# Kernel tuning notes

Measured on AMD Instinct MI355X. Metric: run time of the kernel, lower is better.

Reference implementation:

```python
import jax, jax.numpy as jnp
import numpy as np
from jax import lax

B, L, D, NH, EL, PL, CIN, DFF, NTF = 64, 512, 128, 8, 2, 96, 8, 2048, 4
EPS = 1e-5

def _pos_encoding(seq_len, d):
    pos = np.arange(seq_len, dtype=np.float32)[:, None]
    div = np.exp(np.arange(0, d, 2, dtype=np.float32) * -(np.log(10000.0) / d))
    pe = np.zeros((seq_len, d), dtype=np.float32)
    pe[:, 0::2] = np.sin(pos * div)
    pe[:, 1::2] = np.cos(pos * div)
    return jnp.asarray(pe)

def _layernorm(x, g, b):
    mu = x.mean(-1, keepdims=True)
    var = ((x - mu) ** 2).mean(-1, keepdims=True)
    return (x - mu) * lax.rsqrt(var + EPS) * g + b

def setup_inputs() -> dict:
    key = jax.random.key(0)
    ks = iter(jax.random.split(key, 40))
    s = 0.02
    inp = {
        'x_enc': jax.random.normal(next(ks), (B, L, CIN), jnp.float32),
        'x_mark_enc': jax.random.normal(next(ks), (B, L, NTF), jnp.float32),
        'x_dec': jax.random.normal(next(ks), (B, PL, CIN), jnp.float32),
        'x_mark_dec': jax.random.normal(next(ks), (B, PL, NTF), jnp.float32),
        'conv_w': jax.random.normal(next(ks), (D, CIN, 3), jnp.float32) * s,
        'temp_w': jax.random.normal(next(ks), (D, NTF), jnp.float32) * s,
        'lstm_Wih': jax.random.normal(next(ks), (4 * D, D), jnp.float32) * s,
        'lstm_Whh': jax.random.normal(next(ks), (4 * D, D), jnp.float32) * s,
        'lstm_bih': jnp.zeros((4 * D,), jnp.float32),
        'lstm_bhh': jnp.zeros((4 * D,), jnp.float32),
        'Wqkv': jax.random.normal(next(ks), (EL, 3 * D, D), jnp.float32) * s,
        'bqkv': jnp.zeros((EL, 3 * D), jnp.float32),
        'Wo': jax.random.normal(next(ks), (EL, D, D), jnp.float32) * s,
        'bo': jnp.zeros((EL, D), jnp.float32),
        'ln1g': jnp.ones((EL, D), jnp.float32),
        'ln1b': jnp.zeros((EL, D), jnp.float32),
        'W1': jax.random.normal(next(ks), (EL, DFF, D), jnp.float32) * s,
        'b1': jnp.zeros((EL, DFF), jnp.float32),
        'W2': jax.random.normal(next(ks), (EL, D, DFF), jnp.float32) * s,
        'b2': jnp.zeros((EL, D), jnp.float32),
        'ln2g': jnp.ones((EL, D), jnp.float32),
        'ln2b': jnp.zeros((EL, D), jnp.float32),
        'head_w': jax.random.normal(next(ks), (PL, D), jnp.float32) * s,
        'head_b': jnp.zeros((PL,), jnp.float32),
        'gate_w1': jax.random.normal(next(ks), (D // 2, D), jnp.float32) * s,
        'gate_b1': jnp.zeros((D // 2,), jnp.float32),
        'gate_w2': jax.random.normal(next(ks), (PL, D // 2), jnp.float32) * s,
        'gate_b2': jnp.zeros((PL,), jnp.float32),
        'g_omega': jnp.array([0.01], jnp.float32),
        'g_alpha': jnp.array([-2.0], jnp.float32),
        'g_beta': jnp.array([1.0], jnp.float32),
        'g_h0': jnp.array([0.1], jnp.float32),
    }
    return inp

def reference(x_enc, x_mark_enc, x_dec, x_mark_dec, conv_w, temp_w,
              lstm_Wih, lstm_Whh, lstm_bih, lstm_bhh,
              Wqkv, bqkv, Wo, bo, ln1g, ln1b, W1, b1, W2, b2, ln2g, ln2b,
              head_w, head_b, gate_w1, gate_b1, gate_w2, gate_b2,
              g_omega, g_alpha, g_beta, g_h0):
    # ---- NeuralGARCH: scalar linear recurrence over seq, then pred rollout ----
    returns = x_enc[:, :, -2]                       # [B, L]
    omega = jax.nn.softplus(g_omega[0])
    alpha = jax.nn.sigmoid(g_alpha[0]) * 0.2
    beta = jax.nn.sigmoid(g_beta[0]) * 0.8
    h0 = jnp.broadcast_to(jax.nn.softplus(g_h0[0]), (B,))
    def g_step(h, r):
        return omega + alpha * r ** 2 + beta * h, None
    h_last, _ = lax.scan(g_step, h0, returns.T)     # scan over L
    def f_step(h, _):
        return omega + (alpha + beta) * h, h
    _, hs = lax.scan(f_step, h_last, None, length=PL)   # [PL, B]
    garch_pred = jnp.sqrt(hs.T)                     # [B, PL]
    # ---- DataEmbedding: circular conv1d + temporal linear + positional ----
    xc = jnp.transpose(x_enc, (0, 2, 1))            # [B, CIN, L]
    xp = jnp.pad(xc, ((0, 0), (0, 0), (1, 1)), mode='wrap')
    val = lax.conv_general_dilated(xp, conv_w, (1,), 'VALID',
                                   dimension_numbers=('NCH', 'OIH', 'NCH'))
    val = jnp.transpose(val, (0, 2, 1))             # [B, L, D]
    enc = val + x_mark_enc @ temp_w.T + _pos_encoding(L, D)[None]
    # ---- single-layer LSTM (gate order i,f,g,o) ----
    xW = enc @ lstm_Wih.T + lstm_bih + lstm_bhh     # [B, L, 4D]
    def l_step(carry, xw_t):
        h, c = carry
        g = xw_t + h @ lstm_Whh.T
        i, f, gg, o = jnp.split(g, 4, axis=-1)
        c = jax.nn.sigmoid(f) * c + jax.nn.sigmoid(i) * jnp.tanh(gg)
        h = jax.nn.sigmoid(o) * jnp.tanh(c)
        return (h, c), h
    init = (jnp.zeros((B, D), enc.dtype), jnp.zeros((B, D), enc.dtype))
    _, hseq = lax.scan(l_step, init, jnp.transpose(xW, (1, 0, 2)))
    x = jnp.transpose(hseq, (1, 0, 2))              # [B, L, D]
    # ---- TransformerEncoder (post-norm, relu) ----
    dh = D // NH
    for li in range(EL):
        qkv = x @ Wqkv[li].T + bqkv[li]
        q, k, v = jnp.split(qkv, 3, axis=-1)
        q = q.reshape(B, L, NH, dh).transpose(0, 2, 1, 3)
        k = k.reshape(B, L, NH, dh).transpose(0, 2, 1, 3)
        v = v.reshape(B, L, NH, dh).transpose(0, 2, 1, 3)
        scores = jnp.einsum('bhqd,bhkd->bhqk', q, k) / jnp.sqrt(jnp.float32(dh))
        attn = jax.nn.softmax(scores, axis=-1)
        ctx = jnp.einsum('bhqk,bhkd->bhqd', attn, v)
        ctx = ctx.transpose(0, 2, 1, 3).reshape(B, L, D)
        x = _layernorm(x + ctx @ Wo[li].T + bo[li], ln1g[li], ln1b[li])
        ff = jax.nn.relu(x @ W1[li].T + b1[li]) @ W2[li].T + b2[li]
        x = _layernorm(x + ff, ln2g[li], ln2b[li])
    last = x[:, -1, :]                              # [B, D]
    ai_residual = last @ head_w.T + head_b          # [B, PL]
    gate = jax.nn.sigmoid(jax.nn.relu(last @ gate_w1.T + gate_b1) @ gate_w2.T + gate_b2)
    final = garch_pred + gate * ai_residual
    return final[..., None]                         # [B, PL, 1]
```

## Files before the change

### kernel.cpp

```cpp
#include <hip/hip_runtime.h>
#include <hip/hip_bf16.h>
#include <math.h>

#define Bn 64
#define Lq 512
#define Dm 128
#define NHh 8
#define ELn 2
#define PLn 96
#define CINn 8
#define DFFn 2048
#define NTFn 4
#define EPSf 1e-5f

typedef __attribute__((ext_vector_type(8))) short short8v;
typedef __attribute__((ext_vector_type(4))) float f32x4;

__device__ __forceinline__ short f2b(float f) {
    union { float f; unsigned u; } v; v.f = f;
    unsigned r = v.u + 0x7fff + ((v.u >> 16) & 1);
    return (short)(r >> 16);
}
__device__ __forceinline__ float b2f(short s) {
    union { unsigned u; float f; } v;
    v.u = ((unsigned)(unsigned short)s) << 16;
    return v.f;
}
__device__ __forceinline__ float fsig(float x) {
    return __builtin_amdgcn_rcpf(1.f + __expf(-x));
}
__device__ __forceinline__ float fast_tanh(float x) {
    float ax = fabsf(x);
    float e = __expf(2.f * ax);
    float t = 1.f - 2.f * __builtin_amdgcn_rcpf(e + 1.f);
    return copysignf(t, x);
}
__device__ __forceinline__ void gload_lds16(const short* g, short* l) {
    __builtin_amdgcn_global_load_lds(
        (const __attribute__((address_space(1))) void*)g,
        (__attribute__((address_space(3))) void*)l, 16, 0, 0);
}
__device__ __forceinline__ void gload_lds16f(const float* g, float* l) {
    __builtin_amdgcn_global_load_lds(
        (const __attribute__((address_space(1))) void*)g,
        (__attribute__((address_space(3))) void*)l, 16, 0, 0);
}
__device__ __forceinline__ short8v zero8() {
    short8v z;
#pragma unroll
    for (int e = 0; e < 8; ++e) z[e] = 0;
    return z;
}

__global__ void prep_kernel(const float* __restrict__ Wqkv, const float* __restrict__ Wo,
                            const float* __restrict__ W1, const float* __restrict__ W2,
                            const float* __restrict__ Whh, const float* __restrict__ Wih,
                            const float* __restrict__ bih, const float* __restrict__ bhh,
                            short* __restrict__ Wqkv_b, short* __restrict__ Wo_b,
                            short* __restrict__ W1_b, short* __restrict__ W2_b,
                            short* __restrict__ Whh_b, short* __restrict__ Wih_b,
                            float* __restrict__ biassum)
{
    int i = blockIdx.x * 256 + threadIdx.x;
    if (i < 98304)        Wqkv_b[i] = f2b(Wqkv[i]);
    else if (i < 131072)  { int j = i - 98304;   Wo_b[j]  = f2b(Wo[j]); }
    else if (i < 655360)  { int j = i - 131072;  W1_b[j]  = f2b(W1[j]); }
    else if (i < 1179648) { int j = i - 655360;  W2_b[j]  = f2b(W2[j]); }
    else if (i < 1245184) { int j = i - 1179648; Whh_b[j] = f2b(Whh[j]); }
    else if (i < 1310720) { int j = i - 1245184; Wih_b[j] = f2b(Wih[j]); }
    else if (i < 1311232) { int j = i - 1310720; biassum[j] = bih[j] + bhh[j]; }
}

__global__ void enc_kernel(const float* __restrict__ x_enc,
                           const float* __restrict__ x_mark,
                           const float* __restrict__ conv_w,
                           const float* __restrict__ temp_w,
                           short* __restrict__ encb,
                           const float* __restrict__ g_omega,
                           const float* __restrict__ g_alpha,
                           const float* __restrict__ g_beta,
                           const float* __restrict__ g_h0,
                           float* __restrict__ garch)
{
    int idx = blockIdx.x * blockDim.x + threadIdx.x;
    int d = idx & (Dm - 1);
    int l = (idx >> 7) & (Lq - 1);
    int b = idx >> 16;
    int lm = (l + Lq - 1) & (Lq - 1);
    int lp = (l + 1) & (Lq - 1);
    const float* xb = x_enc + (size_t)b * Lq * CINn;
    const float* w  = conv_w + (size_t)d * CINn * 3;
    float acc = 0.f;
#pragma unroll
    for (int ci = 0; ci < CINn; ++ci) {
        acc += xb[(size_t)lm * CINn + ci] * w[ci * 3 + 0];
        acc += xb[(size_t)l  * CINn + ci] * w[ci * 3 + 1];
        acc += xb[(size_t)lp * CINn + ci] * w[ci * 3 + 2];
    }
    const float* mk = x_mark + ((size_t)b * Lq + l) * NTFn;
    const float* tw = temp_w + (size_t)d * NTFn;
#pragma unroll
    for (int f = 0; f < NTFn; ++f) acc += mk[f] * tw[f];
    float dv = __expf(-(float)(d & ~1) * (9.210340371976184f / 128.f));
    float ang = (float)l * dv;
    acc += (d & 1) ? cosf(ang) : sinf(ang);
    encb[idx] = f2b(acc);

    if (blockIdx.x == 0 && threadIdx.x < Bn) {
        int bb = threadIdx.x;
        float omega = log1pf(__expf(g_omega[0]));
        float alpha = 0.2f / (1.f + __expf(-g_alpha[0]));
        float beta  = 0.8f / (1.f + __expf(-g_beta[0]));
        float h = log1pf(__expf(g_h0[0]));
        const float* xe = x_enc + (size_t)bb * Lq * CINn + (CINn - 2);
        for (int t = 0; t < Lq; ++t) {
            float r = xe[(size_t)t * CINn];
            h = omega + alpha * r * r + beta * h;
        }
        float ab = alpha + beta;
        for (int p = 0; p < PLn; ++p) {
            garch[bb * PLn + p] = sqrtf(h);
            h = omega + ab * h;
        }
    }
}

__global__ __launch_bounds__(256) void gemm_stage(
    const short* __restrict__ A, const short* __restrict__ W,
    const float* __restrict__ b1,
    float* __restrict__ Cf, short* __restrict__ Cb,
    int M, int N, int K, int relu)
{
    __shared__ short As[128 * 128];
    __shared__ short Ws[128 * 128];
    int tid = threadIdx.x;
    int w = tid >> 6, lane = tid & 63;
    int wr = w >> 1, wc = w & 1;
    int m0 = blockIdx.x * 128, n0 = blockIdx.y * 128;
    int lr = lane & 15;
    int lkq = lane >> 4;
    int srow_in = lane >> 4;
    int jp = lane & 15;
    f32x4 acc[4][4] = {};

    for (int k0 = 0; k0 < K; k0 += 128) {
        if (k0) __syncthreads();
#pragma unroll
        for (int inst = 0; inst < 8; ++inst) {
            int c = w * 8 + inst;
            int r = c * 4 + srow_in;
            int j = jp ^ (r & 7);
            gload_lds16(A + (size_t)(m0 + r) * K + k0 + j * 8, &As[c * 512]);
            gload_lds16(W + (size_t)(n0 + r) * K + k0 + j * 8, &Ws[c * 512]);
        }
        __syncthreads();
#pragma unroll
        for (int kq = 0; kq < 4; ++kq) {
            int jlog = kq * 4 + lkq;
            short8v a[4], b[4];
#pragma unroll
            for (int i = 0; i < 4; ++i) {
                int ri = wr * 64 + i * 16 + lr;
                a[i] = *reinterpret_cast<const short8v*>(&As[ri * 128 + (jlog ^ (ri & 7)) * 8]);
            }
#pragma unroll
            for (int jj = 0; jj < 4; ++jj) {
                int rj = wc * 64 + jj * 16 + lr;
                b[jj] = *reinterpret_cast<const short8v*>(&Ws[rj * 128 + (jlog ^ (rj & 7)) * 8]);
            }
#pragma unroll
            for (int i = 0; i < 4; ++i)
#pragma unroll
                for (int jj = 0; jj < 4; ++jj)
                    acc[i][jj] = __builtin_amdgcn_mfma_f32_16x16x32_bf16(
                        a[i], b[jj], acc[i][jj], 0, 0, 0);
        }
    }
    int cr0 = (lane >> 4) * 4;
    int cc = lane & 15;
#pragma unroll
    for (int i = 0; i < 4; ++i)
#pragma unroll
        for (int jj = 0; jj < 4; ++jj) {
            int col = n0 + wc * 64 + jj * 16 + cc;
            float bias = b1[col];
#pragma unroll
            for (int r = 0; r < 4; ++r) {
                int row = m0 + wr * 64 + i * 16 + cr0 + r;
                float v = acc[i][jj][r] + bias;
                if (relu) v = fmaxf(v, 0.f);
                if (Cf) Cf[(size_t)row * N + col] = v;
                else    Cb[(size_t)row * N + col] = f2b(v);
            }
        }
}

__global__ __launch_bounds__(256, 1) void ffn_fused(
    const short* __restrict__ X, const short* __restrict__ W1w,
    const float* __restrict__ bias1,
    const short* __restrict__ W2w, const float* __restrict__ bias2,
    float* __restrict__ out)
{
    __shared__ short Xs[128 * 128];
    __shared__ short Wa[128 * 128];
    __shared__ short Wb[128 * 128];
    __shared__ short Ps[128 * 128];
    int tid = threadIdx.x;
    int w = tid >> 6, lane = tid & 63;
    int wr = w >> 1, wc = w & 1;
    int m0 = blockIdx.x * 128;
    int lr = lane & 15;
    int lkq = lane >> 4;
    int srow_in = lane >> 4;
    int jp = lane & 15;
    int cr0 = (lane >> 4) * 4;
    int cc = lane & 15;

#pragma unroll
    for (int inst = 0; inst < 8; ++inst) {
        int c = w * 8 + inst;
        int r = c * 4 + srow_in;
        int j = jp ^ (r & 7);
        gload_lds16(X + (size_t)(m0 + r) * 128 + j * 8, &Xs[c * 512]);
    }

    f32x4 acc[4][4] = {};
    for (int f = 0; f < 16; ++f) {
#pragma unroll
        for (int inst = 0; inst < 8; ++inst) {
            int c = w * 8 + inst;
            int r = c * 4 + srow_in;
            int j = jp ^ (r & 7);
            gload_lds16(W1w + (size_t)(f * 128 + r) * 128 + j * 8, &Wa[c * 512]);
        }
        __syncthreads();
        float bv[4];
#pragma unroll
        for (int jj = 0; jj < 4; ++jj) bv[jj] = bias1[f * 128 + wc * 64 + jj * 16 + cc];
        f32x4 acc1[4][4] = {};
#pragma unroll
        for (int kq = 0; kq < 4; ++kq) {
            int jlog = kq * 4 + lkq;
            short8v a[4], b[4];
#pragma unroll
            for (int i = 0; i < 4; ++i) {
                int ri = wr * 64 + i * 16 + lr;
                a[i] = *reinterpret_cast<const short8v*>(&Xs[ri * 128 + (jlog ^ (ri & 7)) * 8]);
            }
#pragma unroll
            for (int jj = 0; jj < 4; ++jj) {
                int rj = wc * 64 + jj * 16 + lr;
                b[jj] = *reinterpret_cast<const short8v*>(&Wa[rj * 128 + (jlog ^ (rj & 7)) * 8]);
            }
#pragma unroll
            for (int i = 0; i < 4; ++i)
#pragma unroll
                for (int jj = 0; jj < 4; ++jj)
                    acc1[i][jj] = __builtin_amdgcn_mfma_f32_16x16x32_bf16(
                        a[i], b[jj], acc1[i][jj], 0, 0, 0);
        }
#pragma unroll
        for (int inst = 0; inst < 8; ++inst) {
            int c = w * 8 + inst;
            int r = c * 4 + srow_in;
            int j = jp ^ (r & 7);
            gload_lds16(W2w + (size_t)r * 2048 + f * 128 + j * 8, &Wb[c * 512]);
        }
#pragma unroll
        for (int i = 0; i < 4; ++i)
#pragma unroll
            for (int jj = 0; jj < 4; ++jj) {
                int col = wc * 64 + jj * 16 + cc;
                int jc = col >> 3, ec = col & 7;
#pragma unroll
                for (int r = 0; r < 4; ++r) {
                    int row = wr * 64 + i * 16 + cr0 + r;
                    float v = fmaxf(acc1[i][jj][r] + bv[jj], 0.f);
                    Ps[row * 128 + ((jc ^ (row & 7)) * 8 + ec)] = f2b(v);
                }
            }
        __syncthreads();
#pragma unroll
        for (int kq = 0; kq < 4; ++kq) {
            int jlog = kq * 4 + lkq;
            short8v a[4], b[4];
#pragma unroll
            for (int i = 0; i < 4; ++i) {
                int ri = wr * 64 + i * 16 + lr;
                a[i] = *reinterpret_cast<const short8v*>(&Ps[ri * 128 + (jlog ^ (ri & 7)) * 8]);
            }
#pragma unroll
            for (int jj = 0; jj < 4; ++jj) {
                int rj = wc * 64 + jj * 16 + lr;
                b[jj] = *reinterpret_cast<const short8v*>(&Wb[rj * 128 + (jlog ^ (rj & 7)) * 8]);
            }
#pragma unroll
            for (int i = 0; i < 4; ++i)
#pragma unroll
                for (int jj = 0; jj < 4; ++jj)
                    acc[i][jj] = __builtin_amdgcn_mfma_f32_16x16x32_bf16(
                        a[i], b[jj], acc[i][jj], 0, 0, 0);
        }
    }
#pragma unroll
    for (int i = 0; i < 4; ++i)
#pragma unroll
        for (int jj = 0; jj < 4; ++jj) {
            int col = wc * 64 + jj * 16 + cc;
            float bias = bias2[col];
#pragma unroll
            for (int r = 0; r < 4; ++r) {
                int row = m0 + wr * 64 + i * 16 + cr0 + r;
                out[(size_t)row * Dm + col] = acc[i][jj][r] + bias;
            }
        }
}

__global__ __launch_bounds__(256, 1) void lstm_kernel(
    const float* __restrict__ xW, const short* __restrict__ Whh_b,
    short* __restrict__ xb_out)
{
    __shared__ __align__(16) short hb[2][Dm];
    __shared__ __align__(16) float xs[2][8 * 512];
    int b = blockIdx.x;
    int tid = threadIdx.x;
    int w = tid >> 6;
    int lane = tid & 63;
    int lr = lane & 15;
    int lk = (lane >> 4) * 8;
    int cr0 = (lane >> 4) * 4;
    int qs = lr >> 2;
    int qr = lr & 3;
    int d = w * 32 + qs * 16 + cr0 + qr;
    bool owner = (lr < 8);

    short8v a[4][2][4];
#pragma unroll
    for (int g = 0; g < 4; ++g)
#pragma unroll
        for (int s = 0; s < 2; ++s)
#pragma unroll
            for (int k = 0; k < 4; ++k)
                a[g][s][k] = *reinterpret_cast<const short8v*>(
                    &Whh_b[(size_t)(g * 128 + w * 32 + s * 16 + lr) * Dm + k * 32 + lk]);

    const float* xwb = xW + (size_t)b * Lq * 512;
    auto stage = [&](int c, int buf) {
        const float* src = xwb + (size_t)c * 4096 + w * 1024 + lane * 4;
        float* dst = &xs[buf][w * 1024];
#pragma unroll
        for (int i = 0; i < 4; ++i)
            gload_lds16f(src + i * 256, dst + i * 256);
    };

    float cpers = 0.f;
    if (tid < 64) reinterpret_cast<int*>(hb[0])[tid] = 0;
    stage(0, 0);
    stage(1, 1);

    short* xo = xb_out + (size_t)b * Lq * Dm + d;
    short hsv[8];
    asm volatile("s_waitcnt lgkmcnt(0)" ::: "memory");

    for (int c = 0; c < 64; ++c) {
        int buf = c & 1;
        asm volatile("s_waitcnt vmcnt(4)" ::: "memory");
        __builtin_amdgcn_sched_barrier(0);
        __builtin_amdgcn_s_barrier();
#pragma unroll
        for (int s8 = 0; s8 < 8; ++s8) {
            short8v bf[4];
#pragma unroll
            for (int k = 0; k < 4; ++k)
                bf[k] = *reinterpret_cast<const short8v*>(&hb[s8 & 1][k * 32 + lk]);
            f32x4 acc[4][2] = {};
#pragma unroll
            for (int k = 0; k < 4; ++k)
#pragma unroll
                for (int g = 0; g < 4; ++g)
#pragma unroll
                    for (int s = 0; s < 2; ++s)
                        acc[g][s] = __builtin_amdgcn_mfma_f32_16x16x32_bf16(
                            a[g][s][k], bf[k], acc[g][s], 0, 0, 0);
            if (owner) {
                float iraw = 0.f, fraw = 0.f, graw = 0.f, oraw = 0.f;
#pragma unroll
                for (int s = 0; s < 2; ++s)
#pragma unroll
                    for (int r = 0; r < 4; ++r)
                        if (qs == s && qr == r) {
                            iraw = acc[0][s][r]; fraw = acc[1][s][r];
                            graw = acc[2][s][r]; oraw = acc[3][s][r];
                        }
                iraw += xs[buf][s8 * 512 + 0 * 128 + d];
                fraw += xs[buf][s8 * 512 + 1 * 128 + d];
                graw += xs[buf][s8 * 512 + 2 * 128 + d];
                oraw += xs[buf][s8 * 512 + 3 * 128 + d];
                float ig = fsig(iraw);
                float fg = fsig(fraw);
                float gg = fast_tanh(graw);
                float og = fsig(oraw);
                cpers = fg * cpers + ig * gg;
                float h = og * fast_tanh(cpers);
                short hv = f2b(h);
                hsv[s8] = hv;
                hb[(s8 & 1) ^ 1][d] = hv;
            }
            asm volatile("s_waitcnt lgkmcnt(0)" ::: "memory");
            __builtin_amdgcn_s_barrier();
        }
        int cn = (c + 2 < 64) ? c + 2 : 63;
        stage(cn, buf);
        if (owner) {
#pragma unroll
            for (int s8 = 0; s8 < 8; ++s8)
                xo[(size_t)(c * 8 + s8) * Dm] = hsv[s8];
        }
    }
}

__global__ __launch_bounds__(256, 1) void attn_kernel(
    const short* __restrict__ qkvb, short* __restrict__ ctxb)
{
    __shared__ __align__(16) short Klds[512 * 16];
    __shared__ __align__(16) short Plds[4][16 * 40];
    __shared__ __align__(16) float Flds[4][16];
    int h = blockIdx.x & (NHh - 1);
    int b = blockIdx.x >> 3;
    int tid = threadIdx.x;
    int w = tid >> 6, lane = tid & 63;
    int cc = lane & 15, kg = lane >> 4;
    const short* base = qkvb + (size_t)b * Lq * 384;
    int hoff = h * 16;

    for (int i = tid; i < 1024; i += 256) {
        int r = i >> 1, half = i & 1;
        *reinterpret_cast<short8v*>(&Klds[r * 16 + half * 8]) =
            *reinterpret_cast<const short8v*>(&base[(size_t)r * 384 + 128 + hoff + half * 8]);
    }

    short8v vf[16];
#pragma unroll
    for (int g = 0; g < 16; ++g) {
        short8v v;
#pragma unroll
        for (int e = 0; e < 8; ++e)
            v[e] = base[(size_t)(g * 32 + kg * 8 + e) * 384 + 256 + hoff + cc];
        vf[g] = v;
    }
    __syncthreads();

    int wq0 = w * 128;
    for (int qt = 0; qt < 8; ++qt) {
        short8v qf = zero8();
        if (kg < 2)
            qf = *reinterpret_cast<const short8v*>(
                &base[(size_t)(wq0 + qt * 16 + cc) * 384 + hoff + kg * 8]);
        f32x4 O = {};
        float m = -1e30f, lsum = 0.f;
#pragma unroll
        for (int g = 0; g < 16; ++g) {
#pragma unroll
            for (int half = 0; half < 2; ++half) {
                int kt = g * 2 + half;
                short8v kf = zero8();
                if (kg < 2)
                    kf = *reinterpret_cast<const short8v*>(&Klds[(kt * 16 + cc) * 16 + kg * 8]);
                f32x4 s4 = __builtin_amdgcn_mfma_f32_16x16x32_bf16(kf, qf, f32x4{}, 0, 0, 0);
                float s0 = s4[0] * 0.25f, s1 = s4[1] * 0.25f;
                float s2 = s4[2] * 0.25f, s3 = s4[3] * 0.25f;
                float rmax = fmaxf(fmaxf(s0, s1), fmaxf(s2, s3));
                rmax = fmaxf(rmax, __shfl_xor(rmax, 16));
                rmax = fmaxf(rmax, __shfl_xor(rmax, 32));
                if (__any(rmax > m + 8.f)) {
                    float newm = fmaxf(m, rmax);
                    float fac = __expf(m - newm);
                    m = newm;
                    lsum *= fac;
                    if (kg == 0) Flds[w][cc] = fac;
                    f32x4 fv = *reinterpret_cast<f32x4*>(&Flds[w][kg * 4]);
                    O[0] *= fv[0]; O[1] *= fv[1]; O[2] *= fv[2]; O[3] *= fv[3];
                }
                float p0 = __expf(s0 - m), p1 = __expf(s1 - m);
                float p2 = __expf(s2 - m), p3 = __expf(s3 - m);
                lsum += (p0 + p1) + (p2 + p3);
                uint2 pk;
                pk.x = (unsigned)(unsigned short)f2b(p0) |
                       ((unsigned)(unsigned short)f2b(p1) << 16);
                pk.y = (unsigned)(unsigned short)f2b(p2) |
                       ((unsigned)(unsigned short)f2b(p3) << 16);
                *reinterpret_cast<uint2*>(&Plds[w][cc * 40 + half * 16 + kg * 4]) = pk;
            }
            short8v pf = *reinterpret_cast<const short8v*>(&Plds[w][cc * 40 + kg * 8]);
            O = __builtin_amdgcn_mfma_f32_16x16x32_bf16(pf, vf[g], O, 0, 0, 0);
        }
        lsum += __shfl_xor(lsum, 16);
        lsum += __shfl_xor(lsum, 32);
        float inv = __builtin_amdgcn_rcpf(lsum);
        if (kg == 0) Flds[w][cc] = inv;
        f32x4 iv = *reinterpret_cast<f32x4*>(&Flds[w][kg * 4]);
        int qrow = wq0 + qt * 16 + kg * 4;
        short* o = ctxb + ((size_t)b * Lq + qrow) * Dm + hoff + cc;
#pragma unroll
        for (int r = 0; r < 4; ++r)
            o[(size_t)r * Dm] = f2b(O[r] * iv[r]);
    }
}

__global__ __launch_bounds__(256) void addln_kernel(
    float* __restrict__ x, const short* __restrict__ base_b,
    const float* __restrict__ add,
    const float* __restrict__ g, const float* __restrict__ bta,
    short* __restrict__ xb)
{
    int wave = threadIdx.x >> 6;
    int lane = threadIdx.x & 63;
    int row = blockIdx.x * 4 + wave;
    float* xr = x + (size_t)row * Dm;
    const float* ar = add + (size_t)row * Dm;
    int d0 = lane * 2;
    float b0, b1v;
    if (base_b) {
        unsigned pk = *reinterpret_cast<const unsigned*>(&base_b[(size_t)row * Dm + d0]);
        b0 = b2f((short)(pk & 0xffff));
        b1v = b2f((short)(pk >> 16));
    } else {
        float2 xv = *reinterpret_cast<const float2*>(&xr[d0]);
        b0 = xv.x; b1v = xv.y;
    }
    float2 av = *reinterpret_cast<const float2*>(&ar[d0]);
    float v0 = b0 + av.x, v1 = b1v + av.y;
    float s = v0 + v1;
#pragma unroll
    for (int off = 32; off > 0; off >>= 1) s += __shfl_xor(s, off);
    float mu = s * (1.f / Dm);
    float e0 = v0 - mu, e1 = v1 - mu;
    float s2 = e0 * e0 + e1 * e1;
#pragma unroll
    for (int off = 32; off > 0; off >>= 1) s2 += __shfl_xor(s2, off);
    float rs = rsqrtf(s2 * (1.f / Dm) + EPSf);
    float o0 = e0 * rs * g[d0] + bta[d0];
    float o1 = e1 * rs * g[d0 + 1] + bta[d0 + 1];
    xr[d0] = o0;
    xr[d0 + 1] = o1;
    unsigned pk = (unsigned)(unsigned short)f2b(o0) | ((unsigned)(unsigned short)f2b(o1) << 16);
    *reinterpret_cast<unsigned*>(&xb[(size_t)row * Dm + d0]) = pk;
}

__global__ void head_kernel(const float* __restrict__ x,
                            const float* __restrict__ head_w, const float* __restrict__ head_b,
                            const float* __restrict__ gw1, const float* __restrict__ gb1,
                            const float* __restrict__ gw2, const float* __restrict__ gb2,
                            const float* __restrict__ garch,
                            float* __restrict__ out)
{
    __shared__ float last[Dm];
    __shared__ float t1[Dm / 2];
    int b = blockIdx.x, t = threadIdx.x;
    if (t < Dm) last[t] = x[((size_t)b * Lq + (Lq - 1)) * Dm + t];
    __syncthreads();
    if (t < Dm / 2) {
        float s = gb1[t];
#pragma unroll 8
        for (int d = 0; d < Dm; ++d) s += last[d] * gw1[(size_t)t * Dm + d];
        t1[t] = fmaxf(s, 0.f);
    }
    __syncthreads();
    if (t < PLn) {
        float ai = head_b[t];
#pragma unroll 8
        for (int d = 0; d < Dm; ++d) ai += last[d] * head_w[(size_t)t * Dm + d];
        float gg = gb2[t];
#pragma unroll 8
        for (int j = 0; j < Dm / 2; ++j) gg += t1[j] * gw2[(size_t)t * (Dm / 2) + j];
        float gate = 1.f / (1.f + __expf(-gg));
        out[b * PLn + t] = garch[b * PLn + t] + gate * ai;
    }
}

extern "C" void kernel_launch(void* const* d_in, const int* in_sizes, int n_in,
                              void* d_out, int out_size, void* d_ws, size_t ws_size,
                              hipStream_t stream)
{
    const float* x_enc  = (const float*)d_in[0];
    const float* x_mark = (const float*)d_in[1];
    const float* conv_w = (const float*)d_in[4];
    const float* temp_w = (const float*)d_in[5];
    const float* Wih    = (const float*)d_in[6];
    const float* Whh    = (const float*)d_in[7];
    const float* bih    = (const float*)d_in[8];
    const float* bhh    = (const float*)d_in[9];
    const float* Wqkv   = (const float*)d_in[10];
    const float* bqkv   = (const float*)d_in[11];
    const float* Wo     = (const float*)d_in[12];
    const float* bo     = (const float*)d_in[13];
    const float* ln1g   = (const float*)d_in[14];
    const float* ln1b   = (const float*)d_in[15];
    const float* W1     = (const float*)d_in[16];
    const float* b1     = (const float*)d_in[17];
    const float* W2     = (const float*)d_in[18];
    const float* b2     = (const float*)d_in[19];
    const float* ln2g   = (const float*)d_in[20];
    const float* ln2b   = (const float*)d_in[21];
    const float* head_w = (const float*)d_in[22];
    const float* head_b = (const float*)d_in[23];
    const float* gw1    = (const float*)d_in[24];
    const float* gb1    = (const float*)d_in[25];
    const float* gw2    = (const float*)d_in[26];
    const float* gb2    = (const float*)d_in[27];
    const float* g_omega= (const float*)d_in[28];
    const float* g_alpha= (const float*)d_in[29];
    const float* g_beta = (const float*)d_in[30];
    const float* g_h0   = (const float*)d_in[31];

    const int M = Bn * Lq;
    float* ws    = (float*)d_ws;
    float* garch = ws;
    float* biassum = ws + 6144;
    float* regionA = ws + 8192;
    short* xb   = (short*)regionA;
    short* ctxb = (short*)(regionA + 2097152);
    float* xWr  = regionA + 4194304;
    float* xW   = xWr;
    float* x    = xWr + 16777216;
    float* qkvr = x + 4194304;
    short* encb = (short*)qkvr;
    short* qkvb = (short*)qkvr;
    float* tmp  = qkvr;
    float* wbr  = qkvr + 12582912;
    short* Wqkv_b = (short*)wbr;
    short* Wo_b   = Wqkv_b + 98304;
    short* W1_b   = Wo_b + 32768;
    short* W2_b   = W1_b + 524288;
    short* Whh_bb = W2_b + 524288;
    short* Wih_b  = Whh_bb + 65536;

    prep_kernel<<<5122, 256, 0, stream>>>(Wqkv, Wo, W1, W2, Whh, Wih, bih, bhh,
                                          Wqkv_b, Wo_b, W1_b, W2_b, Whh_bb, Wih_b, biassum);
    enc_kernel<<<(Bn * Lq * Dm) / 256, 256, 0, stream>>>(
        x_enc, x_mark, conv_w, temp_w, encb, g_omega, g_alpha, g_beta, g_h0, garch);
    gemm_stage<<<dim3(M / 128, 512 / 128), 256, 0, stream>>>(
        encb, Wih_b, biassum, xW, nullptr, M, 512, Dm, 0);
    lstm_kernel<<<Bn, 256, 0, stream>>>(xW, Whh_bb, xb);

    for (int li = 0; li < ELn; ++li) {
        gemm_stage<<<dim3(M / 128, 384 / 128), 256, 0, stream>>>(
            xb, Wqkv_b + (size_t)li * 384 * Dm, bqkv + li * 384, nullptr, qkvb, M, 384, Dm, 0);
        attn_kernel<<<Bn * NHh, 256, 0, stream>>>(qkvb, ctxb);
        gemm_stage<<<dim3(M / 128, Dm / 128), 256, 0, stream>>>(
            ctxb, Wo_b + (size_t)li * Dm * Dm, bo + li * Dm, tmp, nullptr, M, Dm, Dm, 0);
        addln_kernel<<<M / 4, 256, 0, stream>>>(
            x, (li == 0) ? xb : nullptr, tmp, ln1g + li * Dm, ln1b + li * Dm, xb);
        ffn_fused<<<M / 128, 256, 0, stream>>>(
            xb, W1_b + (size_t)li * DFFn * Dm, b1 + li * DFFn,
            W2_b + (size_t)li * Dm * DFFn, b2 + li * Dm, tmp);
        addln_kernel<<<M / 4, 256, 0, stream>>>(
            x, nullptr, tmp, ln2g + li * Dm, ln2b + li * Dm, xb);
    }
    head_kernel<<<Bn, 128, 0, stream>>>(x, head_w, head_b, gw1, gb1, gw2, gb2, garch,
                                        (float*)d_out);
}
```

Baseline: 816.5 us.

## Fuse residual add and layernorm into Wo GEMM and FFN epilogues

```diff
diff --git a/kernel.cpp b/kernel.cpp
--- a/kernel.cpp
+++ b/kernel.cpp
@@ -52,6 +52,102 @@
     return z;
 }
 
+__device__ __forceinline__ void ln_epi(
+    f32x4 (&acc)[4][4], int wr, int wc, int lane, int m0,
+    const float* __restrict__ bias, float* __restrict__ x,
+    const short* __restrict__ base_b,
+    const float* __restrict__ g, const float* __restrict__ bta,
+    short* __restrict__ xb, float* redbuf)
+{
+    int cc = lane & 15, q = lane >> 4, cr0 = q * 4;
+    float bvv[4], gv[4], bb[4];
+#pragma unroll
+    for (int jj = 0; jj < 4; ++jj) {
+        int col = wc * 64 + jj * 16 + cc;
+        bvv[jj] = bias[col]; gv[jj] = g[col]; bb[jj] = bta[col];
+    }
+#pragma unroll
+    for (int i = 0; i < 4; ++i)
+#pragma unroll
+        for (int jj = 0; jj < 4; ++jj) {
+            int col = wc * 64 + jj * 16 + cc;
+#pragma unroll
+            for (int r = 0; r < 4; ++r) {
+                int rowg = m0 + wr * 64 + i * 16 + cr0 + r;
+                float resid = base_b ? b2f(base_b[(size_t)rowg * Dm + col])
+                                     : x[(size_t)rowg * Dm + col];
+                acc[i][jj][r] += bvv[jj] + resid;
+            }
+        }
+    int rlb = wr * 64 + cr0;
+    float mu[4][4];
+#pragma unroll
+    for (int i = 0; i < 4; ++i)
+#pragma unroll
+        for (int r = 0; r < 4; ++r) {
+            float s = (acc[i][0][r] + acc[i][1][r]) + (acc[i][2][r] + acc[i][3][r]);
+            s += __shfl_xor(s, 1); s += __shfl_xor(s, 2);
+            s += __shfl_xor(s, 4); s += __shfl_xor(s, 8);
+            mu[i][r] = s;
+        }
+    if (cc == 0) {
+#pragma unroll
+        for (int i = 0; i < 4; ++i)
+#pragma unroll
+            for (int r = 0; r < 4; ++r)
+                redbuf[wc * 128 + rlb + i * 16 + r] = mu[i][r];
+    }
+    __syncthreads();
+#pragma unroll
+    for (int i = 0; i < 4; ++i)
+#pragma unroll
+        for (int r = 0; r < 4; ++r)
+            mu[i][r] = (mu[i][r] + redbuf[(wc ^ 1) * 128 + rlb + i * 16 + r]) * (1.f / 128.f);
+    float rs[4][4];
+#pragma unroll
+    for (int i = 0; i < 4; ++i)
+#pragma unroll
+        for (int r = 0; r < 4; ++r) {
+            float s2 = 0.f;
+#pragma unroll
+            for (int jj = 0; jj < 4; ++jj) {
+                acc[i][jj][r] -= mu[i][r];
+                s2 += acc[i][jj][r] * acc[i][jj][r];
+            }
+            s2 += __shfl_xor(s2, 1); s2 += __shfl_xor(s2, 2);
+            s2 += __shfl_xor(s2, 4); s2 += __shfl_xor(s2, 8);
+            rs[i][r] = s2;
+        }
+    __syncthreads();
+    if (cc == 0) {
+#pragma unroll
+        for (int i = 0; i < 4; ++i)
+#pragma unroll
+            for (int r = 0; r < 4; ++r)
+                redbuf[wc * 128 + rlb + i * 16 + r] = rs[i][r];
+    }
+    __syncthreads();
+#pragma unroll
+    for (int i = 0; i < 4; ++i)
+#pragma unroll
+        for (int r = 0; r < 4; ++r)
+            rs[i][r] = rsqrtf((rs[i][r] + redbuf[(wc ^ 1) * 128 + rlb + i * 16 + r]) *
+                              (1.f / 128.f) + EPSf);
+#pragma unroll
+    for (int i = 0; i < 4; ++i)
+#pragma unroll
+        for (int jj = 0; jj < 4; ++jj) {
+            int col = wc * 64 + jj * 16 + cc;
+#pragma unroll
+            for (int r = 0; r < 4; ++r) {
+                int rowg = m0 + wr * 64 + i * 16 + cr0 + r;
+                float o = acc[i][jj][r] * rs[i][r] * gv[jj] + bb[jj];
+                x[(size_t)rowg * Dm + col] = o;
+                xb[(size_t)rowg * Dm + col] = f2b(o);
+            }
+        }
+}
+
 __global__ void prep_kernel(const float* __restrict__ Wqkv, const float* __restrict__ Wo,
                             const float* __restrict__ W1, const float* __restrict__ W2,
                             const float* __restrict__ Whh, const float* __restrict__ Wih,
@@ -59,7 +155,7 @@
                             short* __restrict__ Wqkv_b, short* __restrict__ Wo_b,
                             short* __restrict__ W1_b, short* __restrict__ W2_b,
                             short* __restrict__ Whh_b, short* __restrict__ Wih_b,
-                            float* __restrict__ biassum)
+                            float* __restrict__ biassum, float* __restrict__ ptab)
 {
     int i = blockIdx.x * 256 + threadIdx.x;
     if (i < 98304)        Wqkv_b[i] = f2b(Wqkv[i]);
@@ -69,6 +165,13 @@
     else if (i < 1245184) { int j = i - 1179648; Whh_b[j] = f2b(Whh[j]); }
     else if (i < 1310720) { int j = i - 1245184; Wih_b[j] = f2b(Wih[j]); }
     else if (i < 1311232) { int j = i - 1310720; biassum[j] = bih[j] + bhh[j]; }
+    else if (i < 1376768) {
+        int j = i - 1311232;
+        int l = j >> 7, d = j & 127;
+        float dv = __expf(-(float)(d & ~1) * (9.210340371976184f / 128.f));
+        float ang = (float)l * dv;
+        ptab[j] = (d & 1) ? cosf(ang) : sinf(ang);
+    }
 }
 
 __global__ void enc_kernel(const float* __restrict__ x_enc,
@@ -76,6 +179,7 @@
                            const float* __restrict__ conv_w,
                            const float* __restrict__ temp_w,
                            short* __restrict__ encb,
+                           const float* __restrict__ ptab,
                            const float* __restrict__ g_omega,
                            const float* __restrict__ g_alpha,
                            const float* __restrict__ g_beta,
@@ -101,9 +205,7 @@
     const float* tw = temp_w + (size_t)d * NTFn;
 #pragma unroll
     for (int f = 0; f < NTFn; ++f) acc += mk[f] * tw[f];
-    float dv = __expf(-(float)(d & ~1) * (9.210340371976184f / 128.f));
-    float ang = (float)l * dv;
-    acc += (d & 1) ? cosf(ang) : sinf(ang);
+    acc += ptab[idx & 65535];
     encb[idx] = f2b(acc);
 
     if (blockIdx.x == 0 && threadIdx.x < Bn) {
@@ -195,16 +297,71 @@
         }
 }
 
-__global__ __launch_bounds__(256, 1) void ffn_fused(
+__global__ __launch_bounds__(256) void gemm_ln(
+    const short* __restrict__ A, const short* __restrict__ W,
+    const float* __restrict__ bias,
+    float* __restrict__ x, const short* __restrict__ base_b,
+    const float* __restrict__ g, const float* __restrict__ bta,
+    short* __restrict__ xb)
+{
+    __shared__ short As[128 * 128];
+    __shared__ short Ws[128 * 128];
+    __shared__ float redbuf[256];
+    int tid = threadIdx.x;
+    int w = tid >> 6, lane = tid & 63;
+    int wr = w >> 1, wc = w & 1;
+    int m0 = blockIdx.x * 128;
+    int lr = lane & 15;
+    int lkq = lane >> 4;
+    int srow_in = lane >> 4;
+    int jp = lane & 15;
+    f32x4 acc[4][4] = {};
+
+#pragma unroll
+    for (int inst = 0; inst < 8; ++inst) {
+        int c = w * 8 + inst;
+        int r = c * 4 + srow_in;
+        int j = jp ^ (r & 7);
+        gload_lds16(A + (size_t)(m0 + r) * 128 + j * 8, &As[c * 512]);
+        gload_lds16(W + (size_t)r * 128 + j * 8, &Ws[c * 512]);
+    }
+    __syncthreads();
+#pragma unroll
+    for (int kq = 0; kq < 4; ++kq) {
+        int jlog = kq * 4 + lkq;
+        short8v a[4], b[4];
+#pragma unroll
+        for (int i = 0; i < 4; ++i) {
+            int ri = wr * 64 + i * 16 + lr;
+            a[i] = *reinterpret_cast<const short8v*>(&As[ri * 128 + (jlog ^ (ri & 7)) * 8]);
+        }
+#pragma unroll
+        for (int jj = 0; jj < 4; ++jj) {
+            int rj = wc * 64 + jj * 16 + lr;
+            b[jj] = *reinterpret_cast<const short8v*>(&Ws[rj * 128 + (jlog ^ (rj & 7)) * 8]);
+        }
+#pragma unroll
+        for (int i = 0; i < 4; ++i)
+#pragma unroll
+            for (int jj = 0; jj < 4; ++jj)
+                acc[i][jj] = __builtin_amdgcn_mfma_f32_16x16x32_bf16(
+                    a[i], b[jj], acc[i][jj], 0, 0, 0);
+    }
+    ln_epi(acc, wr, wc, lane, m0, bias, x, base_b, g, bta, xb, redbuf);
+}
+
+__global__ __launch_bounds__(256, 1) void ffn_ln(
     const short* __restrict__ X, const short* __restrict__ W1w,
     const float* __restrict__ bias1,
     const short* __restrict__ W2w, const float* __restrict__ bias2,
-    float* __restrict__ out)
+    float* __restrict__ x, const float* __restrict__ g,
+    const float* __restrict__ bta, short* __restrict__ xb)
 {
     __shared__ short Xs[128 * 128];
     __shared__ short Wa[128 * 128];
     __shared__ short Wb[128 * 128];
     __shared__ short Ps[128 * 128];
+    __shared__ float redbuf[256];
     int tid = threadIdx.x;
     int w = tid >> 6, lane = tid & 63;
     int wr = w >> 1, wc = w & 1;
@@ -302,18 +459,7 @@
                         a[i], b[jj], acc[i][jj], 0, 0, 0);
         }
     }
-#pragma unroll
-    for (int i = 0; i < 4; ++i)
-#pragma unroll
-        for (int jj = 0; jj < 4; ++jj) {
-            int col = wc * 64 + jj * 16 + cc;
-            float bias = bias2[col];
-#pragma unroll
-            for (int r = 0; r < 4; ++r) {
-                int row = m0 + wr * 64 + i * 16 + cr0 + r;
-                out[(size_t)row * Dm + col] = acc[i][jj][r] + bias;
-            }
-        }
+    ln_epi(acc, wr, wc, lane, m0, bias2, x, nullptr, g, bta, xb, redbuf);
 }
 
 __global__ __launch_bounds__(256, 1) void lstm_kernel(
@@ -505,46 +651,6 @@
         for (int r = 0; r < 4; ++r)
             o[(size_t)r * Dm] = f2b(O[r] * iv[r]);
     }
-}
-
-__global__ __launch_bounds__(256) void addln_kernel(
-    float* __restrict__ x, const short* __restrict__ base_b,
-    const float* __restrict__ add,
-    const float* __restrict__ g, const float* __restrict__ bta,
-    short* __restrict__ xb)
-{
-    int wave = threadIdx.x >> 6;
-    int lane = threadIdx.x & 63;
-    int row = blockIdx.x * 4 + wave;
-    float* xr = x + (size_t)row * Dm;
-    const float* ar = add + (size_t)row * Dm;
-    int d0 = lane * 2;
-    float b0, b1v;
-    if (base_b) {
-        unsigned pk = *reinterpret_cast<const unsigned*>(&base_b[(size_t)row * Dm + d0]);
-        b0 = b2f((short)(pk & 0xffff));
-        b1v = b2f((short)(pk >> 16));
-    } else {
-        float2 xv = *reinterpret_cast<const float2*>(&xr[d0]);
-        b0 = xv.x; b1v = xv.y;
-    }
-    float2 av = *reinterpret_cast<const float2*>(&ar[d0]);
-    float v0 = b0 + av.x, v1 = b1v + av.y;
-    float s = v0 + v1;
-#pragma unroll
-    for (int off = 32; off > 0; off >>= 1) s += __shfl_xor(s, off);
-    float mu = s * (1.f / Dm);
-    float e0 = v0 - mu, e1 = v1 - mu;
-    float s2 = e0 * e0 + e1 * e1;
-#pragma unroll
-    for (int off = 32; off > 0; off >>= 1) s2 += __shfl_xor(s2, off);
-    float rs = rsqrtf(s2 * (1.f / Dm) + EPSf);
-    float o0 = e0 * rs * g[d0] + bta[d0];
-    float o1 = e1 * rs * g[d0 + 1] + bta[d0 + 1];
-    xr[d0] = o0;
-    xr[d0 + 1] = o1;
-    unsigned pk = (unsigned)(unsigned short)f2b(o0) | ((unsigned)(unsigned short)f2b(o1) << 16);
-    *reinterpret_cast<unsigned*>(&xb[(size_t)row * Dm + d0]) = pk;
 }
 
 __global__ void head_kernel(const float* __restrict__ x,
@@ -626,7 +732,7 @@
     float* qkvr = x + 4194304;
     short* encb = (short*)qkvr;
     short* qkvb = (short*)qkvr;
-    float* tmp  = qkvr;
+    float* ptab = qkvr + 8388608;
     float* wbr  = qkvr + 12582912;
     short* Wqkv_b = (short*)wbr;
     short* Wo_b   = Wqkv_b + 98304;
@@ -635,10 +741,11 @@
     short* Whh_bb = W2_b + 524288;
     short* Wih_b  = Whh_bb + 65536;
 
-    prep_kernel<<<5122, 256, 0, stream>>>(Wqkv, Wo, W1, W2, Whh, Wih, bih, bhh,
-                                          Wqkv_b, Wo_b, W1_b, W2_b, Whh_bb, Wih_b, biassum);
+    prep_kernel<<<5378, 256, 0, stream>>>(Wqkv, Wo, W1, W2, Whh, Wih, bih, bhh,
+                                          Wqkv_b, Wo_b, W1_b, W2_b, Whh_bb, Wih_b,
+                                          biassum, ptab);
     enc_kernel<<<(Bn * Lq * Dm) / 256, 256, 0, stream>>>(
-        x_enc, x_mark, conv_w, temp_w, encb, g_omega, g_alpha, g_beta, g_h0, garch);
+        x_enc, x_mark, conv_w, temp_w, encb, ptab, g_omega, g_alpha, g_beta, g_h0, garch);
     gemm_stage<<<dim3(M / 128, 512 / 128), 256, 0, stream>>>(
         encb, Wih_b, biassum, xW, nullptr, M, 512, Dm, 0);
     lstm_kernel<<<Bn, 256, 0, stream>>>(xW, Whh_bb, xb);
@@ -647,15 +754,13 @@
         gemm_stage<<<dim3(M / 128, 384 / 128), 256, 0, stream>>>(
             xb, Wqkv_b + (size_t)li * 384 * Dm, bqkv + li * 384, nullptr, qkvb, M, 384, Dm, 0);
         attn_kernel<<<Bn * NHh, 256, 0, stream>>>(qkvb, ctxb);
-        gemm_stage<<<dim3(M / 128, Dm / 128), 256, 0, stream>>>(
-            ctxb, Wo_b + (size_t)li * Dm * Dm, bo + li * Dm, tmp, nullptr, M, Dm, Dm, 0);
-        addln_kernel<<<M / 4, 256, 0, stream>>>(
-            x, (li == 0) ? xb : nullptr, tmp, ln1g + li * Dm, ln1b + li * Dm, xb);
-        ffn_fused<<<M / 128, 256, 0, stream>>>(
+        gemm_ln<<<M / 128, 256, 0, stream>>>(
+            ctxb, Wo_b + (size_t)li * Dm * Dm, bo + li * Dm,
+            x, (li == 0) ? xb : nullptr, ln1g + li * Dm, ln1b + li * Dm, xb);
+        ffn_ln<<<M / 128, 256, 0, stream>>>(
             xb, W1_b + (size_t)li * DFFn * Dm, b1 + li * DFFn,
-            W2_b + (size_t)li * Dm * DFFn, b2 + li * Dm, tmp);
-        addln_kernel<<<M / 4, 256, 0, stream>>>(
-            x, nullptr, tmp, ln2g + li * Dm, ln2b + li * Dm, xb);
+            W2_b + (size_t)li * Dm * DFFn, b2 + li * Dm,
+            x, ln2g + li * Dm, ln2b + li * Dm, xb);
     }
     head_kernel<<<Bn, 128, 0, stream>>>(x, head_w, head_b, gw1, gb1, gw2, gb2, garch,
                                         (float*)d_out);
```

New measurement: 789.7 us. 3.3% less time.
